# Kernel tuning notes

Hardware: AMD Instinct MI355X
Metric: run time of the kernel (lower is better)

The kernel has to match this reference:

```python
import jax, jax.numpy as jnp
import numpy as np

LN_EPS = 1e-5  # torch nn.LayerNorm default
L2_EPS = 1e-12  # F.normalize default


def layer_norm(x, gamma, beta):
    mu = jnp.mean(x, axis=-1, keepdims=True)
    var = jnp.mean(jnp.square(x - mu), axis=-1, keepdims=True)
    return (x - mu) * jax.lax.rsqrt(var + LN_EPS) * gamma + beta


def l2_normalize(x):
    n = jnp.linalg.norm(x, axis=-1, keepdims=True)
    return x / jnp.maximum(n, L2_EPS)


def setup_inputs() -> dict:
    key = jax.random.key(0)
    k_x, k_mu = jax.random.split(key, 2)
    B, C, H, W = 4, 512, 128, 128
    K, M = 19, 5  # num_classes, num_components_per_class
    x = jax.random.normal(k_x, (B, C, H, W), dtype=jnp.float32)
    means = 0.02 * jax.random.normal(k_mu, (K, M, C), dtype=jnp.float32)  # trunc_normal_(std=0.02)
    diagonal = jnp.ones((K, M, C), dtype=jnp.float32)
    feat_gamma = jnp.ones((C,), dtype=jnp.float32)
    feat_beta = jnp.zeros((C,), dtype=jnp.float32)
    mask_gamma = jnp.ones((K,), dtype=jnp.float32)
    mask_beta = jnp.zeros((K,), dtype=jnp.float32)
    return dict(x=x, means=means, diagonal=diagonal,
                feat_gamma=feat_gamma, feat_beta=feat_beta,
                mask_gamma=mask_gamma, mask_beta=mask_beta)


def reference(x, means, diagonal, feat_gamma, feat_beta, mask_gamma, mask_beta):
    B, C, H, W = x.shape
    K, M, D = means.shape
    # rearrange 'b c h w -> (b h w) c'
    f = jnp.transpose(x, (0, 2, 3, 1)).reshape(-1, C)  # (N, D)
    f = layer_norm(f, feat_gamma, feat_beta)
    f = l2_normalize(f)
    # means are re-normalized in-place each forward
    mu = l2_normalize(means).reshape(K * M, D)          # (P, D), P = K*M
    sigma = diagonal.reshape(K * M, D)                  # diagonal scale (std)
    inv_var = 1.0 / jnp.square(sigma)
    # Mahalanobis distance via quadratic expansion (avoids (N,P,D) intermediate):
    # sum_d ((f - mu)/sigma)^2 = f^2 . iv - 2 f . (mu*iv) + sum(mu^2 * iv)
    q1 = jnp.square(f) @ inv_var.T                      # (N, P)
    q2 = f @ (mu * inv_var).T                           # (N, P)
    q3 = jnp.sum(jnp.square(mu) * inv_var, axis=-1)     # (P,)
    maha = q1 - 2.0 * q2 + q3[None, :]
    log_det = jnp.sum(jnp.log(sigma), axis=-1)          # sum log sigma, (P,)
    half_log2pi = 0.5 * D * jnp.log(2.0 * jnp.pi)
    log_prob = -0.5 * maha - log_det[None, :] - half_log2pi  # (N, P)
    log_prob = log_prob.reshape(-1, K, M)
    m_prob = jnp.max(log_prob, axis=-1)                 # amax over components, (N, K)
    out = layer_norm(m_prob, mask_gamma, mask_beta)
    # rearrange '(b h w) k -> b k h w'
    out_seg = jnp.transpose(out.reshape(B, H, W, K), (0, 3, 1, 2))
    return out_seg
```

## Files before the change

kernel.cpp:

```cpp
#include <hip/hip_runtime.h>
#include <math.h>

#define C_ 512
#define HW_ 16384
#define K_ 19
#define M_ 5
#define P_ 95
#define P2 96
#define TPX 32
#define NBLK 2048
#define HL2PI 470.49652900081467f

typedef __attribute__((ext_vector_type(8))) short short8;
typedef __attribute__((ext_vector_type(4))) int int4v;
typedef __attribute__((ext_vector_type(4))) float float4v;

static __device__ __forceinline__ short f2bf(float f) {
  unsigned u = __builtin_bit_cast(unsigned, f);
  unsigned r = (u + 0x7fffu + ((u >> 16) & 1u)) >> 16;
  return (short)r;
}
static __device__ __forceinline__ float bf2f(short s) {
  return __builtin_bit_cast(float, ((unsigned)(unsigned short)s) << 16);
}

static __device__ __forceinline__ int pk2(float a, float b) {
  int r;
  asm("v_cvt_pk_bf16_f32 %0, %1, %2" : "=v"(r) : "v"(a), "v"(b));
  return r;
}

static __device__ __forceinline__ short8 sq8(short8 a) {
  int4v ai = __builtin_bit_cast(int4v, a);
  int4v ri;
#pragma unroll
  for (int j = 0; j < 4; j++) {
    unsigned u = (unsigned)ai[j];
    float lo = __builtin_bit_cast(float, u << 16);
    float hi = __builtin_bit_cast(float, u & 0xffff0000u);
    ri[j] = pk2(lo * lo, hi * hi);
  }
  return __builtin_bit_cast(short8, ri);
}

__device__ __forceinline__ float block_reduce_sum(float v, volatile float* red) {
#pragma unroll
  for (int o = 32; o; o >>= 1) v += __shfl_down(v, o);
  const int lane = threadIdx.x & 63, wv = threadIdx.x >> 6;
  if (lane == 0) red[wv] = v;
  __syncthreads();
  float r = red[0] + red[1] + red[2] + red[3];
  __syncthreads();
  return r;
}

__global__ __launch_bounds__(256) void prep_kernel(
    const float* __restrict__ means, const float* __restrict__ diag,
    short* __restrict__ wbf, float* __restrict__ cterm) {
  const int p = blockIdx.x;
  const int tid = threadIdx.x;
  __shared__ float red[4];
  if (p >= P_) {
    for (int c = tid; c < C_; c += 256) {
      wbf[p * 1024 + c] = 0;
      wbf[p * 1024 + 512 + c] = 0;
    }
    if (tid == 0) cterm[p] = 0.f;
    return;
  }
  const float* mrow = means + (size_t)p * C_;
  const float* srow = diag + (size_t)p * C_;
  float m0 = mrow[tid], m1 = mrow[tid + 256];
  float ss = block_reduce_sum(m0 * m0 + m1 * m1, red);
  float rden = 1.f / fmaxf(sqrtf(ss), 1e-12f);
  float q3 = 0.f, ld = 0.f;
#pragma unroll
  for (int t = 0; t < 2; t++) {
    int c = tid + t * 256;
    float m = mrow[c], s = srow[c];
    float mu = m * rden;
    float iv = 1.f / (s * s);
    wbf[p * 1024 + c] = f2bf(iv);
    wbf[p * 1024 + 512 + c] = f2bf(mu * iv);
    q3 += mu * mu * iv;
    ld += logf(s);
  }
  q3 = block_reduce_sum(q3, red);
  ld = block_reduce_sum(ld, red);
  if (tid == 0) cterm[p] = -0.5f * q3 - ld - HL2PI;
}

__global__ __launch_bounds__(256) void main_kernel(
    const float* __restrict__ x,
    const float* __restrict__ fg, const float* __restrict__ fb,
    const float* __restrict__ mg, const float* __restrict__ mb,
    const short* __restrict__ wbf, const float* __restrict__ cterm,
    float* __restrict__ out) {
  __shared__ __align__(16) char raw[32768];
  __shared__ float redS[128], redQ[128];
  __shared__ float meanA[TPX], rstdA[TPX], rnA[TPX], rn2A[TPX];
  __shared__ float mean2A[TPX], rstd2A[TPX];
  __shared__ float mpr[TPX * 20];

  const int tid = threadIdx.x;
  const int wv = tid >> 6, lane = tid & 63;
  const int cg = tid >> 3, q = tid & 7;
  const int n0 = blockIdx.x * TPX;
  const int b = n0 >> 14;
  const int rem = n0 & 16383;
  const int h = rem >> 7;
  const int w0 = rem & 127;
  const int c16 = cg * 16;
  const int blkw = (q >> 2) * 16 + (cg >> 1);
  const int sbase = (q & 3) * 2 + (cg & 1);
  const float* xp4 = x + (size_t)b * C_ * HW_ + h * 128 + w0 + q * 4;

  float4v s4 = {0.f, 0.f, 0.f, 0.f}, q4 = {0.f, 0.f, 0.f, 0.f};
#pragma unroll
  for (int hc = 0; hc < 2; hc++) {
    float4v xq[8];
#pragma unroll
    for (int i = 0; i < 8; i++)
      xq[i] = *(const float4v*)(xp4 + (size_t)(c16 + hc * 8 + i) * HW_);
#pragma unroll
    for (int i = 0; i < 8; i++) {
      s4 += xq[i];
      q4 += xq[i] * xq[i];
    }
#pragma unroll
    for (int r = 0; r < 4; r++) {
      int4v pk;
#pragma unroll
      for (int j2 = 0; j2 < 4; j2++) pk[j2] = pk2(xq[2 * j2][r], xq[2 * j2 + 1][r]);
      *(int4v*)(raw + blkw * 1024 + ((hc * 4 + r) * 8 + sbase) * 16) = pk;
    }
  }
#pragma unroll
  for (int o = 8; o < 64; o <<= 1) {
#pragma unroll
    for (int c = 0; c < 4; c++) {
      s4[c] += __shfl_down(s4[c], o);
      q4[c] += __shfl_down(q4[c], o);
    }
  }
  if (lane < 8) {
    *(float4v*)(redS + (wv * 8 + lane) * 4) = s4;
    *(float4v*)(redQ + (wv * 8 + lane) * 4) = q4;
  }
  __syncthreads();
  if (tid < 32) {
    float ss = 0.f, qq = 0.f;
#pragma unroll
    for (int w = 0; w < 4; w++) {
      ss += redS[(w * 8 + (tid >> 2)) * 4 + (tid & 3)];
      qq += redQ[(w * 8 + (tid >> 2)) * 4 + (tid & 3)];
    }
    float mean = ss * (1.f / C_);
    float var = qq * (1.f / C_) - mean * mean;
    meanA[tid] = mean;
    rstdA[tid] = rsqrtf(var + 1e-5f);
  }
  __syncthreads();

  {
    float fga[16], fba[16];
#pragma unroll
    for (int i = 0; i < 4; i++) {
      *(float4v*)(fga + i * 4) = *(const float4v*)(fg + c16 + i * 4);
      *(float4v*)(fba + i * 4) = *(const float4v*)(fb + c16 + i * 4);
    }
    const float4v mean4 = *(const float4v*)(meanA + q * 4);
    const float4v rstd4 = *(const float4v*)(rstdA + q * 4);
    float4v s2 = {0.f, 0.f, 0.f, 0.f};
#pragma unroll
    for (int hc = 0; hc < 2; hc++) {
#pragma unroll
      for (int r = 0; r < 4; r++) {
        char* ad = raw + blkw * 1024 + ((hc * 4 + r) * 8 + sbase) * 16;
        short8 xc = *(short8*)ad;
        const float m = mean4[r], sd = rstd4[r];
        float vv[8];
#pragma unroll
        for (int j = 0; j < 8; j++) {
          float v = fmaf((bf2f(xc[j]) - m) * sd, fga[hc * 8 + j], fba[hc * 8 + j]);
          s2[r] = fmaf(v, v, s2[r]);
          vv[j] = v;
        }
        int4v pk;
#pragma unroll
        for (int j2 = 0; j2 < 4; j2++) pk[j2] = pk2(vv[2 * j2], vv[2 * j2 + 1]);
        *(int4v*)ad = pk;
      }
    }
#pragma unroll
    for (int o = 8; o < 64; o <<= 1) {
#pragma unroll
      for (int c = 0; c < 4; c++) s2[c] += __shfl_down(s2[c], o);
    }
    if (lane < 8) *(float4v*)(redS + (wv * 8 + lane) * 4) = s2;
  }
  __syncthreads();
  if (tid < 32) {
    float ss = 0.f;
#pragma unroll
    for (int w = 0; w < 4; w++) ss += redS[(w * 8 + (tid >> 2)) * 4 + (tid & 3)];
    float rn = 1.f / fmaxf(sqrtf(ss), 1e-12f);
    rnA[tid] = rn;
    rn2A[tid] = rn * rn;
  }
  __syncthreads();

  const int pbase = (wv & 1) * 3;
  const int khalf = wv >> 1;
  const int lm = lane & 15, lk = lane >> 4;
  const int slotR =
      ((((lane >> 4) & 1) * 4 + (lane & 3)) * 8 + ((lane >> 2) & 3) * 2 + ((lane >> 5) & 1)) * 16;
  float4v acc[3][2] = {{}, {}, {}};
  const short* wrow = wbf + (((pbase * 16 + lm) << 10) + (khalf << 9) + (lk << 3));
#pragma unroll 4
  for (int ksl = 0; ksl < 16; ksl++) {
    short8 a0 = *(const short8*)(wrow + ksl * 32);
    short8 a1 = *(const short8*)(wrow + 16384 + ksl * 32);
    short8 a2 = *(const short8*)(wrow + 32768 + ksl * 32);
    short8 b0 = *(const short8*)(raw + ksl * 1024 + slotR);
    short8 b1 = *(const short8*)(raw + (16 + ksl) * 1024 + slotR);
    if (khalf == 0) {
      b0 = sq8(b0);
      b1 = sq8(b1);
    }
    acc[0][0] = __builtin_amdgcn_mfma_f32_16x16x32_bf16(a0, b0, acc[0][0], 0, 0, 0);
    acc[0][1] = __builtin_amdgcn_mfma_f32_16x16x32_bf16(a0, b1, acc[0][1], 0, 0, 0);
    acc[1][0] = __builtin_amdgcn_mfma_f32_16x16x32_bf16(a1, b0, acc[1][0], 0, 0, 0);
    acc[1][1] = __builtin_amdgcn_mfma_f32_16x16x32_bf16(a1, b1, acc[1][1], 0, 0, 0);
    acc[2][0] = __builtin_amdgcn_mfma_f32_16x16x32_bf16(a2, b0, acc[2][0], 0, 0, 0);
    acc[2][1] = __builtin_amdgcn_mfma_f32_16x16x32_bf16(a2, b1, acc[2][1], 0, 0, 0);
  }
  __syncthreads();
  float* lp = (float*)raw;

  if (khalf == 0) {
#pragma unroll
    for (int i = 0; i < 3; i++) {
      const int prow = (pbase + i) * 16 + lk * 4;
#pragma unroll
      for (int r = 0; r < 4; r++) {
        const float ct = cterm[prow + r];
#pragma unroll
        for (int t2 = 0; t2 < 2; t2++) {
          const int pxx = t2 * 16 + lm;
          lp[pxx * 100 + prow + r] = fmaf(-0.5f * rn2A[pxx], acc[i][t2][r], ct);
        }
      }
    }
  }
  __syncthreads();
  if (khalf == 1) {
#pragma unroll
    for (int i = 0; i < 3; i++) {
      const int prow = (pbase + i) * 16 + lk * 4;
#pragma unroll
      for (int r = 0; r < 4; r++) {
#pragma unroll
        for (int t2 = 0; t2 < 2; t2++) {
          const int pxx = t2 * 16 + lm;
          lp[pxx * 100 + prow + r] += rnA[pxx] * acc[i][t2][r];
        }
      }
    }
  }
  __syncthreads();

  for (int idx = tid; idx < TPX * K_; idx += 256) {
    const int pxx = idx / K_;
    const int k = idx - pxx * K_;
    const float* row = lp + pxx * 100 + k * M_;
    float mv = row[0];
#pragma unroll
    for (int m = 1; m < M_; m++) mv = fmaxf(mv, row[m]);
    mpr[pxx * 20 + k] = mv;
  }
  __syncthreads();
  if (tid < 32) {
    float ss = 0.f;
    for (int k = 0; k < K_; k++) ss += mpr[tid * 20 + k];
    float m2 = ss * (1.f / K_);
    float qq = 0.f;
    for (int k = 0; k < K_; k++) {
      float d = mpr[tid * 20 + k] - m2;
      qq += d * d;
    }
    mean2A[tid] = m2;
    rstd2A[tid] = rsqrtf(qq * (1.f / K_) + 1e-5f);
  }
  __syncthreads();
  float* obase = out + ((size_t)(b * K_) * 128 + h) * 128 + w0;
  for (int idx = tid; idx < TPX * K_; idx += 256) {
    const int k = idx >> 5, pxx = idx & 31;
    float v = fmaf((mpr[pxx * 20 + k] - mean2A[pxx]) * rstd2A[pxx], mg[k], mb[k]);
    obase[(size_t)k * HW_ + pxx] = v;
  }
}

extern "C" void kernel_launch(void* const* d_in, const int* in_sizes, int n_in,
                              void* d_out, int out_size, void* d_ws, size_t ws_size,
                              hipStream_t stream) {
  const float* x = (const float*)d_in[0];
  const float* means = (const float*)d_in[1];
  const float* diag = (const float*)d_in[2];
  const float* fg = (const float*)d_in[3];
  const float* fb = (const float*)d_in[4];
  const float* mg = (const float*)d_in[5];
  const float* mb = (const float*)d_in[6];
  float* out = (float*)d_out;

  short* wbf = (short*)d_ws;
  float* cterm = (float*)((char*)d_ws + (size_t)P2 * 1024 * 2);

  prep_kernel<<<P2, 256, 0, stream>>>(means, diag, wbf, cterm);
  main_kernel<<<NBLK, 256, 0, stream>>>(x, fg, fb, mg, mb, wbf, cterm, out);
}
```

Measured before the change: 69.44 us.

## Process two pixel tiles per block with register prefetch of next tile

Each block now handles two 32-pixel tiles in sequence and halves the grid. While the current tile's LayerNorm, GEMM and epilogue run, the next tile's x slice is loaded into registers, which is meant to hide global load latency. Per-block constants (gamma, beta, cterm, mask params) are staged in shared memory once per block. Launch bounds request 4 blocks per CU. The prefetch costs 64 extra VGPRs per thread and fewer blocks in flight, which may reduce occupancy.

Result: slower. 78.32 us (+12.8%).

```diff
diff --git a/kernel.cpp b/kernel.cpp
--- a/kernel.cpp
+++ b/kernel.cpp
@@ -8,7 +8,8 @@
 #define P_ 95
 #define P2 96
 #define TPX 32
-#define NBLK 2048
+#define GRID_ 1024
+#define TILES_ 2
 #define HL2PI 470.49652900081467f
 
 typedef __attribute__((ext_vector_type(8))) short short8;
@@ -90,7 +91,7 @@
   if (tid == 0) cterm[p] = -0.5f * q3 - ld - HL2PI;
 }
 
-__global__ __launch_bounds__(256) void main_kernel(
+__global__ __launch_bounds__(256, 4) void main_kernel(
     const float* __restrict__ x,
     const float* __restrict__ fg, const float* __restrict__ fb,
     const float* __restrict__ mg, const float* __restrict__ mb,
@@ -100,204 +101,233 @@
   __shared__ float redS[128], redQ[128];
   __shared__ float meanA[TPX], rstdA[TPX], rnA[TPX], rn2A[TPX];
   __shared__ float mean2A[TPX], rstd2A[TPX];
-  __shared__ float mpr[TPX * 20];
+  __shared__ float fgs[C_], fbs[C_], cts[P2], mgs[K_ + 1], mbs[K_ + 1];
 
   const int tid = threadIdx.x;
   const int wv = tid >> 6, lane = tid & 63;
   const int cg = tid >> 3, q = tid & 7;
-  const int n0 = blockIdx.x * TPX;
-  const int b = n0 >> 14;
-  const int rem = n0 & 16383;
-  const int h = rem >> 7;
-  const int w0 = rem & 127;
   const int c16 = cg * 16;
   const int blkw = (q >> 2) * 16 + (cg >> 1);
   const int sbase = (q & 3) * 2 + (cg & 1);
-  const float* xp4 = x + (size_t)b * C_ * HW_ + h * 128 + w0 + q * 4;
-
-  float4v s4 = {0.f, 0.f, 0.f, 0.f}, q4 = {0.f, 0.f, 0.f, 0.f};
-#pragma unroll
-  for (int hc = 0; hc < 2; hc++) {
-    float4v xq[8];
-#pragma unroll
-    for (int i = 0; i < 8; i++)
-      xq[i] = *(const float4v*)(xp4 + (size_t)(c16 + hc * 8 + i) * HW_);
-#pragma unroll
-    for (int i = 0; i < 8; i++) {
-      s4 += xq[i];
-      q4 += xq[i] * xq[i];
-    }
-#pragma unroll
-    for (int r = 0; r < 4; r++) {
-      int4v pk;
-#pragma unroll
-      for (int j2 = 0; j2 < 4; j2++) pk[j2] = pk2(xq[2 * j2][r], xq[2 * j2 + 1][r]);
-      *(int4v*)(raw + blkw * 1024 + ((hc * 4 + r) * 8 + sbase) * 16) = pk;
-    }
-  }
-#pragma unroll
-  for (int o = 8; o < 64; o <<= 1) {
-#pragma unroll
-    for (int c = 0; c < 4; c++) {
-      s4[c] += __shfl_down(s4[c], o);
-      q4[c] += __shfl_down(q4[c], o);
-    }
-  }
-  if (lane < 8) {
-    *(float4v*)(redS + (wv * 8 + lane) * 4) = s4;
-    *(float4v*)(redQ + (wv * 8 + lane) * 4) = q4;
-  }
-  __syncthreads();
-  if (tid < 32) {
-    float ss = 0.f, qq = 0.f;
-#pragma unroll
-    for (int w = 0; w < 4; w++) {
-      ss += redS[(w * 8 + (tid >> 2)) * 4 + (tid & 3)];
-      qq += redQ[(w * 8 + (tid >> 2)) * 4 + (tid & 3)];
-    }
-    float mean = ss * (1.f / C_);
-    float var = qq * (1.f / C_) - mean * mean;
-    meanA[tid] = mean;
-    rstdA[tid] = rsqrtf(var + 1e-5f);
-  }
-  __syncthreads();
-
+
+  for (int i = tid; i < C_; i += 256) { fgs[i] = fg[i]; fbs[i] = fb[i]; }
+  if (tid < P2) cts[tid] = cterm[tid];
+  if (tid < K_) { mgs[tid] = mg[tid]; mbs[tid] = mb[tid]; }
+
+  float4v pf[16];
   {
-    float fga[16], fba[16];
-#pragma unroll
-    for (int i = 0; i < 4; i++) {
-      *(float4v*)(fga + i * 4) = *(const float4v*)(fg + c16 + i * 4);
-      *(float4v*)(fba + i * 4) = *(const float4v*)(fb + c16 + i * 4);
-    }
-    const float4v mean4 = *(const float4v*)(meanA + q * 4);
-    const float4v rstd4 = *(const float4v*)(rstdA + q * 4);
-    float4v s2 = {0.f, 0.f, 0.f, 0.f};
-#pragma unroll
-    for (int hc = 0; hc < 2; hc++) {
-#pragma unroll
-      for (int r = 0; r < 4; r++) {
-        char* ad = raw + blkw * 1024 + ((hc * 4 + r) * 8 + sbase) * 16;
-        short8 xc = *(short8*)ad;
-        const float m = mean4[r], sd = rstd4[r];
-        float vv[8];
-#pragma unroll
-        for (int j = 0; j < 8; j++) {
-          float v = fmaf((bf2f(xc[j]) - m) * sd, fga[hc * 8 + j], fba[hc * 8 + j]);
-          s2[r] = fmaf(v, v, s2[r]);
-          vv[j] = v;
-        }
-        int4v pk;
-#pragma unroll
-        for (int j2 = 0; j2 < 4; j2++) pk[j2] = pk2(vv[2 * j2], vv[2 * j2 + 1]);
-        *(int4v*)ad = pk;
-      }
-    }
-#pragma unroll
-    for (int o = 8; o < 64; o <<= 1) {
-#pragma unroll
-      for (int c = 0; c < 4; c++) s2[c] += __shfl_down(s2[c], o);
-    }
-    if (lane < 8) *(float4v*)(redS + (wv * 8 + lane) * 4) = s2;
-  }
-  __syncthreads();
-  if (tid < 32) {
-    float ss = 0.f;
-#pragma unroll
-    for (int w = 0; w < 4; w++) ss += redS[(w * 8 + (tid >> 2)) * 4 + (tid & 3)];
-    float rn = 1.f / fmaxf(sqrtf(ss), 1e-12f);
-    rnA[tid] = rn;
-    rn2A[tid] = rn * rn;
-  }
-  __syncthreads();
-
-  const int pbase = (wv & 1) * 3;
-  const int khalf = wv >> 1;
-  const int lm = lane & 15, lk = lane >> 4;
-  const int slotR =
-      ((((lane >> 4) & 1) * 4 + (lane & 3)) * 8 + ((lane >> 2) & 3) * 2 + ((lane >> 5) & 1)) * 16;
-  float4v acc[3][2] = {{}, {}, {}};
-  const short* wrow = wbf + (((pbase * 16 + lm) << 10) + (khalf << 9) + (lk << 3));
+    const int n0 = blockIdx.x * TILES_ * TPX;
+    const int b0 = n0 >> 14, rem = n0 & 16383, h0 = rem >> 7, w00 = rem & 127;
+    const float* xp4 = x + (size_t)b0 * C_ * HW_ + h0 * 128 + w00 + q * 4;
+#pragma unroll
+    for (int i = 0; i < 16; i++)
+      pf[i] = *(const float4v*)(xp4 + (size_t)(c16 + i) * HW_);
+  }
+
+#pragma unroll
+  for (int t = 0; t < TILES_; ++t) {
+    const int n0 = (blockIdx.x * TILES_ + t) * TPX;
+    const int b = n0 >> 14;
+    const int rem = n0 & 16383;
+    const int h = rem >> 7;
+    const int w0 = rem & 127;
+
+    {
+      float4v s4 = {0.f, 0.f, 0.f, 0.f}, q4 = {0.f, 0.f, 0.f, 0.f};
+#pragma unroll
+      for (int i = 0; i < 16; i++) {
+        s4 += pf[i];
+        q4 += pf[i] * pf[i];
+      }
+#pragma unroll
+      for (int hc = 0; hc < 2; hc++) {
+#pragma unroll
+        for (int r = 0; r < 4; r++) {
+          int4v pk;
+#pragma unroll
+          for (int j2 = 0; j2 < 4; j2++)
+            pk[j2] = pk2(pf[hc * 8 + 2 * j2][r], pf[hc * 8 + 2 * j2 + 1][r]);
+          *(int4v*)(raw + blkw * 1024 + ((hc * 4 + r) * 8 + sbase) * 16) = pk;
+        }
+      }
+#pragma unroll
+      for (int o = 8; o < 64; o <<= 1) {
+#pragma unroll
+        for (int c = 0; c < 4; c++) {
+          s4[c] += __shfl_down(s4[c], o);
+          q4[c] += __shfl_down(q4[c], o);
+        }
+      }
+      if (lane < 8) {
+        *(float4v*)(redS + (wv * 8 + lane) * 4) = s4;
+        *(float4v*)(redQ + (wv * 8 + lane) * 4) = q4;
+      }
+    }
+
+    if (t + 1 < TILES_) {
+      const int n0n = (blockIdx.x * TILES_ + t + 1) * TPX;
+      const int bn = n0n >> 14, remn = n0n & 16383, hn = remn >> 7, w0n = remn & 127;
+      const float* xp4n = x + (size_t)bn * C_ * HW_ + hn * 128 + w0n + q * 4;
+#pragma unroll
+      for (int i = 0; i < 16; i++)
+        pf[i] = *(const float4v*)(xp4n + (size_t)(c16 + i) * HW_);
+    }
+    __builtin_amdgcn_sched_barrier(0);
+
+    __syncthreads();
+    if (tid < 32) {
+      float ss = 0.f, qq = 0.f;
+#pragma unroll
+      for (int w = 0; w < 4; w++) {
+        ss += redS[(w * 8 + (tid >> 2)) * 4 + (tid & 3)];
+        qq += redQ[(w * 8 + (tid >> 2)) * 4 + (tid & 3)];
+      }
+      float mean = ss * (1.f / C_);
+      float var = qq * (1.f / C_) - mean * mean;
+      meanA[tid] = mean;
+      rstdA[tid] = rsqrtf(var + 1e-5f);
+    }
+    __syncthreads();
+
+    {
+      float fga[16], fba[16];
+#pragma unroll
+      for (int i = 0; i < 4; i++) {
+        *(float4v*)(fga + i * 4) = *(const float4v*)(fgs + c16 + i * 4);
+        *(float4v*)(fba + i * 4) = *(const float4v*)(fbs + c16 + i * 4);
+      }
+      const float4v mean4 = *(const float4v*)(meanA + q * 4);
+      const float4v rstd4 = *(const float4v*)(rstdA + q * 4);
+      float4v s2 = {0.f, 0.f, 0.f, 0.f};
+#pragma unroll
+      for (int hc = 0; hc < 2; hc++) {
+#pragma unroll
+        for (int r = 0; r < 4; r++) {
+          char* ad = raw + blkw * 1024 + ((hc * 4 + r) * 8 + sbase) * 16;
+          short8 xc = *(short8*)ad;
+          const float m = mean4[r], sd = rstd4[r];
+          float vv[8];
+#pragma unroll
+          for (int j = 0; j < 8; j++) {
+            float v = fmaf((bf2f(xc[j]) - m) * sd, fga[hc * 8 + j], fba[hc * 8 + j]);
+            s2[r] = fmaf(v, v, s2[r]);
+            vv[j] = v;
+          }
+          int4v pk;
+#pragma unroll
+          for (int j2 = 0; j2 < 4; j2++) pk[j2] = pk2(vv[2 * j2], vv[2 * j2 + 1]);
+          *(int4v*)ad = pk;
+        }
+      }
+#pragma unroll
+      for (int o = 8; o < 64; o <<= 1) {
+#pragma unroll
+        for (int c = 0; c < 4; c++) s2[c] += __shfl_down(s2[c], o);
+      }
+      if (lane < 8) *(float4v*)(redS + (wv * 8 + lane) * 4) = s2;
+    }
+    __syncthreads();
+    if (tid < 32) {
+      float ss = 0.f;
+#pragma unroll
+      for (int w = 0; w < 4; w++) ss += redS[(w * 8 + (tid >> 2)) * 4 + (tid & 3)];
+      float rn = 1.f / fmaxf(sqrtf(ss), 1e-12f);
+      rnA[tid] = rn;
+      rn2A[tid] = rn * rn;
+    }
+    __syncthreads();
+
+    const int pbase = (wv & 1) * 3;
+    const int khalf = wv >> 1;
+    const int lm = lane & 15, lk = lane >> 4;
+    const int slotR =
+        ((((lane >> 4) & 1) * 4 + (lane & 3)) * 8 + ((lane >> 2) & 3) * 2 + ((lane >> 5) & 1)) * 16;
+    float4v acc[3][2] = {{}, {}, {}};
+    const short* wrow = wbf + (((pbase * 16 + lm) << 10) + (khalf << 9) + (lk << 3));
 #pragma unroll 4
-  for (int ksl = 0; ksl < 16; ksl++) {
-    short8 a0 = *(const short8*)(wrow + ksl * 32);
-    short8 a1 = *(const short8*)(wrow + 16384 + ksl * 32);
-    short8 a2 = *(const short8*)(wrow + 32768 + ksl * 32);
-    short8 b0 = *(const short8*)(raw + ksl * 1024 + slotR);
-    short8 b1 = *(const short8*)(raw + (16 + ksl) * 1024 + slotR);
+    for (int ksl = 0; ksl < 16; ksl++) {
+      short8 a0 = *(const short8*)(wrow + ksl * 32);
+      short8 a1 = *(const short8*)(wrow + 16384 + ksl * 32);
+      short8 a2 = *(const short8*)(wrow + 32768 + ksl * 32);
+      short8 b0 = *(const short8*)(raw + ksl * 1024 + slotR);
+      short8 b1 = *(const short8*)(raw + (16 + ksl) * 1024 + slotR);
+      if (khalf == 0) {
+        b0 = sq8(b0);
+        b1 = sq8(b1);
+      }
+      acc[0][0] = __builtin_amdgcn_mfma_f32_16x16x32_bf16(a0, b0, acc[0][0], 0, 0, 0);
+      acc[0][1] = __builtin_amdgcn_mfma_f32_16x16x32_bf16(a0, b1, acc[0][1], 0, 0, 0);
+      acc[1][0] = __builtin_amdgcn_mfma_f32_16x16x32_bf16(a1, b0, acc[1][0], 0, 0, 0);
+      acc[1][1] = __builtin_amdgcn_mfma_f32_16x16x32_bf16(a1, b1, acc[1][1], 0, 0, 0);
+      acc[2][0] = __builtin_amdgcn_mfma_f32_16x16x32_bf16(a2, b0, acc[2][0], 0, 0, 0);
+      acc[2][1] = __builtin_amdgcn_mfma_f32_16x16x32_bf16(a2, b1, acc[2][1], 0, 0, 0);
+    }
+    __syncthreads();
+    float* lp = (float*)raw;
+    float* mpr = (float*)(raw + 16384);
+
     if (khalf == 0) {
-      b0 = sq8(b0);
-      b1 = sq8(b1);
-    }
-    acc[0][0] = __builtin_amdgcn_mfma_f32_16x16x32_bf16(a0, b0, acc[0][0], 0, 0, 0);
-    acc[0][1] = __builtin_amdgcn_mfma_f32_16x16x32_bf16(a0, b1, acc[0][1], 0, 0, 0);
-    acc[1][0] = __builtin_amdgcn_mfma_f32_16x16x32_bf16(a1, b0, acc[1][0], 0, 0, 0);
-    acc[1][1] = __builtin_amdgcn_mfma_f32_16x16x32_bf16(a1, b1, acc[1][1], 0, 0, 0);
-    acc[2][0] = __builtin_amdgcn_mfma_f32_16x16x32_bf16(a2, b0, acc[2][0], 0, 0, 0);
-    acc[2][1] = __builtin_amdgcn_mfma_f32_16x16x32_bf16(a2, b1, acc[2][1], 0, 0, 0);
-  }
-  __syncthreads();
-  float* lp = (float*)raw;
-
-  if (khalf == 0) {
-#pragma unroll
-    for (int i = 0; i < 3; i++) {
-      const int prow = (pbase + i) * 16 + lk * 4;
-#pragma unroll
-      for (int r = 0; r < 4; r++) {
-        const float ct = cterm[prow + r];
-#pragma unroll
-        for (int t2 = 0; t2 < 2; t2++) {
-          const int pxx = t2 * 16 + lm;
-          lp[pxx * 100 + prow + r] = fmaf(-0.5f * rn2A[pxx], acc[i][t2][r], ct);
-        }
-      }
-    }
-  }
-  __syncthreads();
-  if (khalf == 1) {
-#pragma unroll
-    for (int i = 0; i < 3; i++) {
-      const int prow = (pbase + i) * 16 + lk * 4;
-#pragma unroll
-      for (int r = 0; r < 4; r++) {
-#pragma unroll
-        for (int t2 = 0; t2 < 2; t2++) {
-          const int pxx = t2 * 16 + lm;
-          lp[pxx * 100 + prow + r] += rnA[pxx] * acc[i][t2][r];
-        }
-      }
-    }
-  }
-  __syncthreads();
-
-  for (int idx = tid; idx < TPX * K_; idx += 256) {
-    const int pxx = idx / K_;
-    const int k = idx - pxx * K_;
-    const float* row = lp + pxx * 100 + k * M_;
-    float mv = row[0];
-#pragma unroll
-    for (int m = 1; m < M_; m++) mv = fmaxf(mv, row[m]);
-    mpr[pxx * 20 + k] = mv;
-  }
-  __syncthreads();
-  if (tid < 32) {
-    float ss = 0.f;
-    for (int k = 0; k < K_; k++) ss += mpr[tid * 20 + k];
-    float m2 = ss * (1.f / K_);
-    float qq = 0.f;
-    for (int k = 0; k < K_; k++) {
-      float d = mpr[tid * 20 + k] - m2;
-      qq += d * d;
-    }
-    mean2A[tid] = m2;
-    rstd2A[tid] = rsqrtf(qq * (1.f / K_) + 1e-5f);
-  }
-  __syncthreads();
-  float* obase = out + ((size_t)(b * K_) * 128 + h) * 128 + w0;
-  for (int idx = tid; idx < TPX * K_; idx += 256) {
-    const int k = idx >> 5, pxx = idx & 31;
-    float v = fmaf((mpr[pxx * 20 + k] - mean2A[pxx]) * rstd2A[pxx], mg[k], mb[k]);
-    obase[(size_t)k * HW_ + pxx] = v;
+#pragma unroll
+      for (int i = 0; i < 3; i++) {
+        const int prow = (pbase + i) * 16 + lk * 4;
+#pragma unroll
+        for (int r = 0; r < 4; r++) {
+          const float ct = cts[prow + r];
+#pragma unroll
+          for (int t2 = 0; t2 < 2; t2++) {
+            const int pxx = t2 * 16 + lm;
+            lp[pxx * 100 + prow + r] = fmaf(-0.5f * rn2A[pxx], acc[i][t2][r], ct);
+          }
+        }
+      }
+    }
+    __syncthreads();
+    if (khalf == 1) {
+#pragma unroll
+      for (int i = 0; i < 3; i++) {
+        const int prow = (pbase + i) * 16 + lk * 4;
+#pragma unroll
+        for (int r = 0; r < 4; r++) {
+#pragma unroll
+          for (int t2 = 0; t2 < 2; t2++) {
+            const int pxx = t2 * 16 + lm;
+            lp[pxx * 100 + prow + r] += rnA[pxx] * acc[i][t2][r];
+          }
+        }
+      }
+    }
+    __syncthreads();
+
+    for (int idx = tid; idx < TPX * K_; idx += 256) {
+      const int pxx = idx / K_;
+      const int k = idx - pxx * K_;
+      const float* row = lp + pxx * 100 + k * M_;
+      float mv = row[0];
+#pragma unroll
+      for (int m = 1; m < M_; m++) mv = fmaxf(mv, row[m]);
+      mpr[pxx * 20 + k] = mv;
+    }
+    __syncthreads();
+    if (tid < 32) {
+      float ss = 0.f;
+      for (int k = 0; k < K_; k++) ss += mpr[tid * 20 + k];
+      float m2 = ss * (1.f / K_);
+      float qq = 0.f;
+      for (int k = 0; k < K_; k++) {
+        float d = mpr[tid * 20 + k] - m2;
+        qq += d * d;
+      }
+      mean2A[tid] = m2;
+      rstd2A[tid] = rsqrtf(qq * (1.f / K_) + 1e-5f);
+    }
+    __syncthreads();
+    float* obase = out + ((size_t)(b * K_) * 128 + h) * 128 + w0;
+    for (int idx = tid; idx < TPX * K_; idx += 256) {
+      const int k = idx >> 5, pxx = idx & 31;
+      float v = fmaf((mpr[pxx * 20 + k] - mean2A[pxx]) * rstd2A[pxx], mgs[k], mbs[k]);
+      obase[(size_t)k * HW_ + pxx] = v;
+    }
+    __syncthreads();
   }
 }
 
@@ -317,5 +347,5 @@
   float* cterm = (float*)((char*)d_ws + (size_t)P2 * 1024 * 2);
 
   prep_kernel<<<P2, 256, 0, stream>>>(means, diag, wbf, cterm);
-  main_kernel<<<NBLK, 256, 0, stream>>>(x, fg, fb, mg, mb, wbf, cterm, out);
-}
+  main_kernel<<<GRID_, 256, 0, stream>>>(x, fg, fb, mg, mb, wbf, cterm, out);
+}
```

## Split main kernel into producer/consumer waves with triple-buffered LDS pipeline

Applied to the files above, without the earlier changes.

Rewrites the main kernel as a persistent 512-thread block. Half the waves load x tiles from global memory into a rotating triple buffer in LDS while the other half normalize and run the MFMA work on the previous half-tile. Each block now handles 4 pixel tiles in half-channel phases, and the grid shrinks from 2048 blocks to 512. The goal is to overlap global loads with compute. The cost is many more block-wide barriers, only half the threads doing math, and higher LDS use per block, which may reduce occupancy.

Result: slower. 126.9 us (+82.7%).

```diff
diff --git a/kernel.cpp b/kernel.cpp
--- a/kernel.cpp
+++ b/kernel.cpp
@@ -7,8 +7,8 @@
 #define M_ 5
 #define P_ 95
 #define P2 96
-#define TPX 32
-#define NBLK 2048
+#define TILES_ 4
+#define GRID_ 512
 #define HL2PI 470.49652900081467f
 
 typedef __attribute__((ext_vector_type(8))) short short8;
@@ -23,13 +23,11 @@
 static __device__ __forceinline__ float bf2f(short s) {
   return __builtin_bit_cast(float, ((unsigned)(unsigned short)s) << 16);
 }
-
 static __device__ __forceinline__ int pk2(float a, float b) {
   int r;
   asm("v_cvt_pk_bf16_f32 %0, %1, %2" : "=v"(r) : "v"(a), "v"(b));
   return r;
 }
-
 static __device__ __forceinline__ short8 sq8(short8 a) {
   int4v ai = __builtin_bit_cast(int4v, a);
   int4v ri;
@@ -90,214 +88,226 @@
   if (tid == 0) cterm[p] = -0.5f * q3 - ld - HL2PI;
 }
 
-__global__ __launch_bounds__(256) void main_kernel(
+__global__ __launch_bounds__(512, 4) void main_kernel(
     const float* __restrict__ x,
     const float* __restrict__ fg, const float* __restrict__ fb,
     const float* __restrict__ mg, const float* __restrict__ mb,
     const short* __restrict__ wbf, const float* __restrict__ cterm,
     float* __restrict__ out) {
-  __shared__ __align__(16) char raw[32768];
-  __shared__ float redS[128], redQ[128];
-  __shared__ float meanA[TPX], rstdA[TPX], rnA[TPX], rn2A[TPX];
-  __shared__ float mean2A[TPX], rstd2A[TPX];
-  __shared__ float mpr[TPX * 20];
+  __shared__ __align__(16) char ubuf[3 * 16384];
+  __shared__ float lp[32 * 100];
+  __shared__ float mpr[32 * 20];
+  __shared__ float redS[128], redQ[128], redV[128];
+  __shared__ float meanA[32], rstdA[32], rnA[32], rn2A[32];
+  __shared__ float mean2A[32], rstd2A[32];
 
   const int tid = threadIdx.x;
-  const int wv = tid >> 6, lane = tid & 63;
-  const int cg = tid >> 3, q = tid & 7;
-  const int n0 = blockIdx.x * TPX;
-  const int b = n0 >> 14;
-  const int rem = n0 & 16383;
-  const int h = rem >> 7;
-  const int w0 = rem & 127;
-  const int c16 = cg * 16;
-  const int blkw = (q >> 2) * 16 + (cg >> 1);
-  const int sbase = (q & 3) * 2 + (cg & 1);
-  const float* xp4 = x + (size_t)b * C_ * HW_ + h * 128 + w0 + q * 4;
-
-  float4v s4 = {0.f, 0.f, 0.f, 0.f}, q4 = {0.f, 0.f, 0.f, 0.f};
-#pragma unroll
-  for (int hc = 0; hc < 2; hc++) {
-    float4v xq[8];
-#pragma unroll
-    for (int i = 0; i < 8; i++)
-      xq[i] = *(const float4v*)(xp4 + (size_t)(c16 + hc * 8 + i) * HW_);
-#pragma unroll
-    for (int i = 0; i < 8; i++) {
-      s4 += xq[i];
-      q4 += xq[i] * xq[i];
-    }
-#pragma unroll
-    for (int r = 0; r < 4; r++) {
-      int4v pk;
-#pragma unroll
-      for (int j2 = 0; j2 < 4; j2++) pk[j2] = pk2(xq[2 * j2][r], xq[2 * j2 + 1][r]);
-      *(int4v*)(raw + blkw * 1024 + ((hc * 4 + r) * 8 + sbase) * 16) = pk;
-    }
-  }
-#pragma unroll
-  for (int o = 8; o < 64; o <<= 1) {
-#pragma unroll
-    for (int c = 0; c < 4; c++) {
-      s4[c] += __shfl_down(s4[c], o);
-      q4[c] += __shfl_down(q4[c], o);
-    }
-  }
-  if (lane < 8) {
-    *(float4v*)(redS + (wv * 8 + lane) * 4) = s4;
-    *(float4v*)(redQ + (wv * 8 + lane) * 4) = q4;
-  }
-  __syncthreads();
-  if (tid < 32) {
-    float ss = 0.f, qq = 0.f;
-#pragma unroll
-    for (int w = 0; w < 4; w++) {
-      ss += redS[(w * 8 + (tid >> 2)) * 4 + (tid & 3)];
-      qq += redQ[(w * 8 + (tid >> 2)) * 4 + (tid & 3)];
-    }
-    float mean = ss * (1.f / C_);
-    float var = qq * (1.f / C_) - mean * mean;
-    meanA[tid] = mean;
-    rstdA[tid] = rsqrtf(var + 1e-5f);
-  }
-  __syncthreads();
-
-  {
-    float fga[16], fba[16];
-#pragma unroll
-    for (int i = 0; i < 4; i++) {
-      *(float4v*)(fga + i * 4) = *(const float4v*)(fg + c16 + i * 4);
-      *(float4v*)(fba + i * 4) = *(const float4v*)(fb + c16 + i * 4);
-    }
-    const float4v mean4 = *(const float4v*)(meanA + q * 4);
-    const float4v rstd4 = *(const float4v*)(rstdA + q * 4);
-    float4v s2 = {0.f, 0.f, 0.f, 0.f};
-#pragma unroll
-    for (int hc = 0; hc < 2; hc++) {
-#pragma unroll
-      for (int r = 0; r < 4; r++) {
-        char* ad = raw + blkw * 1024 + ((hc * 4 + r) * 8 + sbase) * 16;
-        short8 xc = *(short8*)ad;
-        const float m = mean4[r], sd = rstd4[r];
-        float vv[8];
-#pragma unroll
-        for (int j = 0; j < 8; j++) {
-          float v = fmaf((bf2f(xc[j]) - m) * sd, fga[hc * 8 + j], fba[hc * 8 + j]);
-          s2[r] = fmaf(v, v, s2[r]);
-          vv[j] = v;
-        }
-        int4v pk;
-#pragma unroll
-        for (int j2 = 0; j2 < 4; j2++) pk[j2] = pk2(vv[2 * j2], vv[2 * j2 + 1]);
-        *(int4v*)ad = pk;
-      }
-    }
-#pragma unroll
-    for (int o = 8; o < 64; o <<= 1) {
-#pragma unroll
-      for (int c = 0; c < 4; c++) s2[c] += __shfl_down(s2[c], o);
-    }
-    if (lane < 8) *(float4v*)(redS + (wv * 8 + lane) * 4) = s2;
-  }
-  __syncthreads();
-  if (tid < 32) {
-    float ss = 0.f;
-#pragma unroll
-    for (int w = 0; w < 4; w++) ss += redS[(w * 8 + (tid >> 2)) * 4 + (tid & 3)];
-    float rn = 1.f / fmaxf(sqrtf(ss), 1e-12f);
-    rnA[tid] = rn;
-    rn2A[tid] = rn * rn;
-  }
-  __syncthreads();
-
-  const int pbase = (wv & 1) * 3;
-  const int khalf = wv >> 1;
+  const bool isProd = tid >= 256;
+  const int rt = tid & 255;
+  const int q = rt & 7, cgr = rt >> 3;
+  const int rw = rt >> 6;
+  const int lane = tid & 63;
+  const int phalf = rw & 1, pxt = rw >> 1;
   const int lm = lane & 15, lk = lane >> 4;
   const int slotR =
       ((((lane >> 4) & 1) * 4 + (lane & 3)) * 8 + ((lane >> 2) & 3) * 2 + ((lane >> 5) & 1)) * 16;
-  float4v acc[3][2] = {{}, {}, {}};
-  const short* wrow = wbf + (((pbase * 16 + lm) << 10) + (khalf << 9) + (lk << 3));
-#pragma unroll 4
-  for (int ksl = 0; ksl < 16; ksl++) {
-    short8 a0 = *(const short8*)(wrow + ksl * 32);
-    short8 a1 = *(const short8*)(wrow + 16384 + ksl * 32);
-    short8 a2 = *(const short8*)(wrow + 32768 + ksl * 32);
-    short8 b0 = *(const short8*)(raw + ksl * 1024 + slotR);
-    short8 b1 = *(const short8*)(raw + (16 + ksl) * 1024 + slotR);
-    if (khalf == 0) {
-      b0 = sq8(b0);
-      b1 = sq8(b1);
-    }
-    acc[0][0] = __builtin_amdgcn_mfma_f32_16x16x32_bf16(a0, b0, acc[0][0], 0, 0, 0);
-    acc[0][1] = __builtin_amdgcn_mfma_f32_16x16x32_bf16(a0, b1, acc[0][1], 0, 0, 0);
-    acc[1][0] = __builtin_amdgcn_mfma_f32_16x16x32_bf16(a1, b0, acc[1][0], 0, 0, 0);
-    acc[1][1] = __builtin_amdgcn_mfma_f32_16x16x32_bf16(a1, b1, acc[1][1], 0, 0, 0);
-    acc[2][0] = __builtin_amdgcn_mfma_f32_16x16x32_bf16(a2, b0, acc[2][0], 0, 0, 0);
-    acc[2][1] = __builtin_amdgcn_mfma_f32_16x16x32_bf16(a2, b1, acc[2][1], 0, 0, 0);
-  }
-  __syncthreads();
-  float* lp = (float*)raw;
-
-  if (khalf == 0) {
-#pragma unroll
-    for (int i = 0; i < 3; i++) {
-      const int prow = (pbase + i) * 16 + lk * 4;
+  const int blkoff = ((q >> 2) * 8 + (cgr >> 2)) * 1024;
+  const int sb = (q & 3) * 2 + ((cgr >> 1) & 1);
+
+  float4v s4, q4, s2v;
+  float4v aQ1[3], aQ2[3];
+  s4[0] = s4[1] = s4[2] = s4[3] = 0.f;
+  q4[0] = q4[1] = q4[2] = q4[3] = 0.f;
+  s2v[0] = s2v[1] = s2v[2] = s2v[3] = 0.f;
+#pragma unroll
+  for (int i = 0; i < 3; i++) {
+#pragma unroll
+    for (int r = 0; r < 4; r++) {
+      aQ1[i][r] = 0.f;
+      aQ2[i][r] = 0.f;
+    }
+  }
+
+#pragma unroll 1
+  for (int ph = 0; ph < 2 * TILES_ + 2; ++ph) {
+    const int sP = ph % 3;
+    const int sC = (ph + 1) % 3;
+    const bool pv = ph < 2 * TILES_;
+    const int tp = ph >> 1, hp = ph & 1;
+    const bool cv = ph >= 2;
+    const int phc = ph - 2;
+    const int tc = phc >> 1, hc2 = phc & 1;
+
+    if (isProd && pv) {
+      const int n0 = (blockIdx.x * TILES_ + tp) * 32;
+      const int bb = n0 >> 14, rem = n0 & 16383, hh = rem >> 7, w0 = rem & 127;
+      const int c0 = hp * 256 + cgr * 8;
+      const float* xp4 = x + (size_t)bb * C_ * HW_ + hh * 128 + w0 + q * 4;
+      float4v xq[8];
+#pragma unroll
+      for (int j = 0; j < 8; j++) xq[j] = *(const float4v*)(xp4 + (size_t)(c0 + j) * HW_);
+#pragma unroll
+      for (int j = 0; j < 8; j++) {
+        s4 += xq[j];
+        q4 += xq[j] * xq[j];
+      }
+      char* buf = ubuf + sP * 16384;
 #pragma unroll
       for (int r = 0; r < 4; r++) {
-        const float ct = cterm[prow + r];
-#pragma unroll
-        for (int t2 = 0; t2 < 2; t2++) {
-          const int pxx = t2 * 16 + lm;
-          lp[pxx * 100 + prow + r] = fmaf(-0.5f * rn2A[pxx], acc[i][t2][r], ct);
-        }
-      }
-    }
-  }
-  __syncthreads();
-  if (khalf == 1) {
-#pragma unroll
-    for (int i = 0; i < 3; i++) {
-      const int prow = (pbase + i) * 16 + lk * 4;
+        int4v pk;
+#pragma unroll
+        for (int j2 = 0; j2 < 4; j2++) pk[j2] = pk2(xq[2 * j2][r], xq[2 * j2 + 1][r]);
+        *(int4v*)(buf + blkoff + (((cgr & 1) * 4 + r) * 8 + sb) * 16) = pk;
+      }
+      if (hp == 1) {
+#pragma unroll
+        for (int o = 8; o < 64; o <<= 1) {
+#pragma unroll
+          for (int c = 0; c < 4; c++) {
+            s4[c] += __shfl_down(s4[c], o);
+            q4[c] += __shfl_down(q4[c], o);
+          }
+        }
+        if (lane < 8) {
+          *(float4v*)(redS + (rw * 8 + lane) * 4) = s4;
+          *(float4v*)(redQ + (rw * 8 + lane) * 4) = q4;
+        }
+        s4[0] = s4[1] = s4[2] = s4[3] = 0.f;
+        q4[0] = q4[1] = q4[2] = q4[3] = 0.f;
+      }
+    }
+    if (!isProd && cv && hc2 == 0 && tid < 32) {
+      float ss = 0.f, qq = 0.f;
+#pragma unroll
+      for (int w = 0; w < 4; w++) {
+        ss += redS[(w * 8 + (tid >> 2)) * 4 + (tid & 3)];
+        qq += redQ[(w * 8 + (tid >> 2)) * 4 + (tid & 3)];
+      }
+      float mean = ss * (1.f / C_);
+      float var = qq * (1.f / C_) - mean * mean;
+      meanA[tid] = mean;
+      rstdA[tid] = rsqrtf(var + 1e-5f);
+    }
+    __syncthreads();
+
+    if (!isProd && cv) {
+      char* buf = ubuf + sC * 16384;
+      const int c0 = hc2 * 256 + cgr * 8;
+      float fga[8], fba[8];
+      *(float4v*)(fga) = *(const float4v*)(fg + c0);
+      *(float4v*)(fga + 4) = *(const float4v*)(fg + c0 + 4);
+      *(float4v*)(fba) = *(const float4v*)(fb + c0);
+      *(float4v*)(fba + 4) = *(const float4v*)(fb + c0 + 4);
 #pragma unroll
       for (int r = 0; r < 4; r++) {
-#pragma unroll
-        for (int t2 = 0; t2 < 2; t2++) {
-          const int pxx = t2 * 16 + lm;
-          lp[pxx * 100 + prow + r] += rnA[pxx] * acc[i][t2][r];
-        }
-      }
-    }
-  }
-  __syncthreads();
-
-  for (int idx = tid; idx < TPX * K_; idx += 256) {
-    const int pxx = idx / K_;
-    const int k = idx - pxx * K_;
-    const float* row = lp + pxx * 100 + k * M_;
-    float mv = row[0];
-#pragma unroll
-    for (int m = 1; m < M_; m++) mv = fmaxf(mv, row[m]);
-    mpr[pxx * 20 + k] = mv;
-  }
-  __syncthreads();
-  if (tid < 32) {
-    float ss = 0.f;
-    for (int k = 0; k < K_; k++) ss += mpr[tid * 20 + k];
-    float m2 = ss * (1.f / K_);
-    float qq = 0.f;
-    for (int k = 0; k < K_; k++) {
-      float d = mpr[tid * 20 + k] - m2;
-      qq += d * d;
-    }
-    mean2A[tid] = m2;
-    rstd2A[tid] = rsqrtf(qq * (1.f / K_) + 1e-5f);
-  }
-  __syncthreads();
-  float* obase = out + ((size_t)(b * K_) * 128 + h) * 128 + w0;
-  for (int idx = tid; idx < TPX * K_; idx += 256) {
-    const int k = idx >> 5, pxx = idx & 31;
-    float v = fmaf((mpr[pxx * 20 + k] - mean2A[pxx]) * rstd2A[pxx], mg[k], mb[k]);
-    obase[(size_t)k * HW_ + pxx] = v;
+        char* ad = buf + blkoff + (((cgr & 1) * 4 + r) * 8 + sb) * 16;
+        short8 xc = *(short8*)ad;
+        const int px = q * 4 + r;
+        const float m = meanA[px], sd = rstdA[px];
+        float vv[8];
+#pragma unroll
+        for (int j = 0; j < 8; j++) {
+          float v = fmaf((bf2f(xc[j]) - m) * sd, fga[j], fba[j]);
+          s2v[r] = fmaf(v, v, s2v[r]);
+          vv[j] = v;
+        }
+        int4v pk;
+#pragma unroll
+        for (int j2 = 0; j2 < 4; j2++) pk[j2] = pk2(vv[2 * j2], vv[2 * j2 + 1]);
+        *(int4v*)ad = pk;
+      }
+    }
+    __syncthreads();
+
+    if (!isProd && cv) {
+      char* buf = ubuf + sC * 16384;
+#pragma unroll 2
+      for (int ksl = 0; ksl < 8; ksl++) {
+        const int ks = hc2 * 8 + ksl;
+        short8 b0 = *(const short8*)(buf + (pxt * 8 + ksl) * 1024 + slotR);
+        short8 b2 = sq8(b0);
+#pragma unroll
+        for (int i = 0; i < 3; i++) {
+          const short* wr = wbf + (((phalf * 3 + i) * 16 + lm) << 10) + (lk << 3) + ks * 32;
+          short8 aiv = *(const short8*)(wr);
+          short8 amv = *(const short8*)(wr + 512);
+          aQ1[i] = __builtin_amdgcn_mfma_f32_16x16x32_bf16(aiv, b2, aQ1[i], 0, 0, 0);
+          aQ2[i] = __builtin_amdgcn_mfma_f32_16x16x32_bf16(amv, b0, aQ2[i], 0, 0, 0);
+        }
+      }
+      if (hc2 == 1) {
+#pragma unroll
+        for (int o = 8; o < 64; o <<= 1) {
+#pragma unroll
+          for (int c = 0; c < 4; c++) s2v[c] += __shfl_down(s2v[c], o);
+        }
+        if (lane < 8) *(float4v*)(redV + (rw * 8 + lane) * 4) = s2v;
+        s2v[0] = s2v[1] = s2v[2] = s2v[3] = 0.f;
+      }
+    }
+    __syncthreads();
+
+    if (cv && hc2 == 1) {
+      if (tid < 32) {
+        float ss = 0.f;
+#pragma unroll
+        for (int w = 0; w < 4; w++) ss += redV[(w * 8 + (tid >> 2)) * 4 + (tid & 3)];
+        float rn = 1.f / fmaxf(sqrtf(ss), 1e-12f);
+        rnA[tid] = rn;
+        rn2A[tid] = rn * rn;
+      }
+      __syncthreads();
+      if (!isProd) {
+        const int pxx = pxt * 16 + lm;
+        const float rn = rnA[pxx], rn2 = rn2A[pxx];
+#pragma unroll
+        for (int i = 0; i < 3; i++) {
+#pragma unroll
+          for (int r = 0; r < 4; r++) {
+            const int p = (phalf * 3 + i) * 16 + lk * 4 + r;
+            lp[pxx * 100 + p] =
+                fmaf(-0.5f * rn2, aQ1[i][r], fmaf(rn, aQ2[i][r], cterm[p]));
+            aQ1[i][r] = 0.f;
+            aQ2[i][r] = 0.f;
+          }
+        }
+      }
+      __syncthreads();
+      for (int idx = tid; idx < 32 * K_; idx += 512) {
+        const int pxx = idx / K_;
+        const int k = idx - pxx * K_;
+        const float* row = lp + pxx * 100 + k * M_;
+        float mv = row[0];
+#pragma unroll
+        for (int m = 1; m < M_; m++) mv = fmaxf(mv, row[m]);
+        mpr[pxx * 20 + k] = mv;
+      }
+      __syncthreads();
+      if (tid < 32) {
+        float ss = 0.f;
+        for (int k = 0; k < K_; k++) ss += mpr[tid * 20 + k];
+        float m2 = ss * (1.f / K_);
+        float qq = 0.f;
+        for (int k = 0; k < K_; k++) {
+          float d = mpr[tid * 20 + k] - m2;
+          qq += d * d;
+        }
+        mean2A[tid] = m2;
+        rstd2A[tid] = rsqrtf(qq * (1.f / K_) + 1e-5f);
+      }
+      __syncthreads();
+      {
+        const int n0c = (blockIdx.x * TILES_ + tc) * 32;
+        const int bc = n0c >> 14, remc = n0c & 16383, hh2 = remc >> 7, w0c = remc & 127;
+        float* obase = out + ((size_t)(bc * K_) * 128 + hh2) * 128 + w0c;
+        for (int idx = tid; idx < 32 * K_; idx += 512) {
+          const int k = idx >> 5, pxx = idx & 31;
+          float v = fmaf((mpr[pxx * 20 + k] - mean2A[pxx]) * rstd2A[pxx], mg[k], mb[k]);
+          obase[(size_t)k * HW_ + pxx] = v;
+        }
+      }
+    }
+    __syncthreads();
   }
 }
 
@@ -317,5 +327,5 @@
   float* cterm = (float*)((char*)d_ws + (size_t)P2 * 1024 * 2);
 
   prep_kernel<<<P2, 256, 0, stream>>>(means, diag, wbf, cterm);
-  main_kernel<<<NBLK, 256, 0, stream>>>(x, fg, fb, mg, mb, wbf, cterm, out);
-}
+  main_kernel<<<GRID_, 512, 0, stream>>>(x, fg, fb, mg, mb, wbf, cterm, out);
+}
```
